# Kernel tuning notes

Measured on AMD Instinct MI355X. Metric: run time of the kernel, lower is better.

Reference implementation:

```python
import jax, jax.numpy as jnp
import numpy as np
import math

N_MENTIONS = 8192
EMB = 1024


def setup_inputs() -> dict:
    key = jax.random.key(0)
    k0, k1, k2 = jax.random.split(key, 3)
    scale = 1.0 / math.sqrt(EMB)
    return {
        "all_mentions": jax.random.normal(k0, (N_MENTIONS, EMB), dtype=jnp.float32),
        "Wq": jax.random.normal(k1, (EMB, EMB), dtype=jnp.float32) * scale,
        "bq": jnp.zeros((EMB,), dtype=jnp.float32),
        "Wk": jax.random.normal(k2, (EMB, EMB), dtype=jnp.float32) * scale,
        "bk": jnp.zeros((EMB,), dtype=jnp.float32),
    }


def reference(all_mentions, Wq, bq, Wk, bk):
    # torch.nn.Linear: y = x @ W.T + b
    E = all_mentions.shape[-1]
    q = (all_mentions @ Wq.T + bq) / jnp.sqrt(jnp.asarray(E, all_mentions.dtype))
    k = all_mentions @ Wk.T + bk
    # [N, N] raw attention logits
    attn = q @ k.T
    # causal mask: -inf strictly above the diagonal (triu, diagonal=1)
    n = all_mentions.shape[0]
    mask = jnp.where(jnp.triu(jnp.ones((n, n), dtype=bool), k=1),
                     jnp.asarray(-jnp.inf, attn.dtype),
                     jnp.asarray(0.0, attn.dtype))
    # Module returns attn_weights = masked pre-softmax logits (single layer,
    # single head, bsz=1); the softmax@v branch is discarded by the caller.
    return attn + mask
```

## Files before the change

kernel.cpp:

```cpp
#include <hip/hip_runtime.h>
#include <math.h>

#define NM 8192
#define KDIM 1024

#define NEG_BIG (-3.0e38f)

typedef __attribute__((ext_vector_type(4))) float floatx4;
typedef __attribute__((ext_vector_type(8))) _Float16 halfx8;
typedef __attribute__((ext_vector_type(4))) _Float16 halfx4;

__device__ __forceinline__ void gload_lds16(const void* g, void* l) {
    __builtin_amdgcn_global_load_lds(
        (const __attribute__((address_space(1))) void*)g,
        (__attribute__((address_space(3))) void*)l,
        16, 0, 0);
}

__global__ __launch_bounds__(256)
void convert_kernel(const float* __restrict__ X,
                    const float* __restrict__ Wq,
                    const float* __restrict__ Wk,
                    _Float16* __restrict__ Xf,
                    _Float16* __restrict__ Wqf,
                    _Float16* __restrict__ Wkf) {
    const int XB = (NM * KDIM) / 4 / 256;
    const int WB = (KDIM * KDIM) / 4 / 256;
    int b = blockIdx.x;
    const float* src;
    _Float16* dst;
    if (b < XB)            { src = X;  dst = Xf; }
    else if (b < XB + WB)  { b -= XB;       src = Wq; dst = Wqf; }
    else                   { b -= XB + WB;  src = Wk; dst = Wkf; }
    const int i = b * 256 + threadIdx.x;
    floatx4 v = ((const floatx4*)src)[i];
    halfx4 h;
    h.x = (_Float16)v.x;
    h.y = (_Float16)v.y;
    h.z = (_Float16)v.z;
    h.w = (_Float16)v.w;
    *(halfx4*)&dst[(size_t)i * 4] = h;
}


__global__ __launch_bounds__(256, 2)
void proj_kernel(const _Float16* __restrict__ Xf,
                 const _Float16* __restrict__ Wqf, const float* __restrict__ bq,
                 _Float16* __restrict__ Qf,
                 const _Float16* __restrict__ Wkf, const float* __restrict__ bk,
                 _Float16* __restrict__ Kf) {
    const bool isK = (blockIdx.z == 1);
    const _Float16* W    = isK ? Wkf : Wqf;
    const float*    bias = isK ? bk : bq;
    _Float16*       O    = isK ? Kf : Qf;
    const float scale = isK ? 1.0f : 0.03125f;

    __shared__ __attribute__((aligned(16))) _Float16 sA[256 * 64];
    __shared__ __attribute__((aligned(16))) _Float16 sB[128 * 64];

    const int t = threadIdx.x;
    const int lane = t & 63;
    const int quad = lane >> 4;
    const int l15 = lane & 15;
    const int wave = t >> 6;
    const int wr = (wave & 1) * 128;
    const int wc = (wave >> 1) * 64;

    const int row0 = blockIdx.y * 256;
    const int col0 = blockIdx.x * 128;

    const int srow = t >> 3;
    const int skoff = (((t & 7) ^ ((t >> 3) & 7)) * 8);

    floatx4 zero = {0.f, 0.f, 0.f, 0.f};
    floatx4 acc[8][4];
#pragma unroll
    for (int i = 0; i < 8; i++)
#pragma unroll
        for (int j = 0; j < 4; j++) acc[i][j] = zero;

    for (int k0 = 0; k0 < KDIM; k0 += 64) {
#pragma unroll
        for (int c = 0; c < 8; c++) {
            const int r = c * 32 + srow;
            const size_t ga = (size_t)(row0 + r) * KDIM + k0 + skoff;
            gload_lds16(Xf + ga, &sA[(c * 256 + t) * 8]);
        }
#pragma unroll
        for (int c = 0; c < 4; c++) {
            const int r = c * 32 + srow;
            const size_t gb = (size_t)(col0 + r) * KDIM + k0 + skoff;
            gload_lds16(W + gb, &sB[(c * 256 + t) * 8]);
        }
        __syncthreads();

#pragma unroll
        for (int kk = 0; kk < 2; kk++) {
            halfx8 a[8];
#pragma unroll
            for (int i = 0; i < 8; i++) {
                const int r = wr + i * 16 + l15;
                const int sl = (kk * 4 + quad) ^ (r & 7);
                a[i] = *(const halfx8*)&sA[r * 64 + sl * 8];
            }
#pragma unroll
            for (int j = 0; j < 4; j++) {
                const int r = wc + j * 16 + l15;
                const int sl = (kk * 4 + quad) ^ (r & 7);
                halfx8 b = *(const halfx8*)&sB[r * 64 + sl * 8];
#pragma unroll
                for (int i = 0; i < 8; i++)
                    acc[i][j] = __builtin_amdgcn_mfma_f32_16x16x32_f16(a[i], b, acc[i][j], 0, 0, 0);
            }
        }
        __syncthreads();
    }

#pragma unroll
    for (int i = 0; i < 8; i++)
#pragma unroll
        for (int j = 0; j < 4; j++)
#pragma unroll
            for (int r = 0; r < 4; r++) {
                const int grow = row0 + wr + i * 16 + quad * 4 + r;
                const int gcol = col0 + wc + j * 16 + l15;
                const float v = (acc[i][j][r] + bias[gcol]) * scale;
                O[(size_t)grow * KDIM + gcol] = (_Float16)v;
            }
}

__global__ __launch_bounds__(256, 2)
void attn_kernel(const _Float16* __restrict__ Qf,
                 const _Float16* __restrict__ Kf,
                 float* __restrict__ out) {
    const int lid = blockIdx.x;
    const int x = lid & 7;
    const int s = lid >> 3;
    const int bi = s & 31;
    const int bj = ((s >> 5) << 3) + x;
    const int t = threadIdx.x;

    if (bj * 128 > bi * 256 + 255) {
        const floatx4 v = {NEG_BIG, NEG_BIG, NEG_BIG, NEG_BIG};
        floatx4* o4 = (floatx4*)(out + (size_t)bi * 256 * NM + (size_t)bj * 128);
#pragma unroll
        for (int it = 0; it < 32; ++it) {
            const int idx = it * 256 + t;
            const int r = idx >> 5;
            const int c = idx & 31;
            __builtin_nontemporal_store(v, &o4[(size_t)r * (NM / 4) + c]);
        }
        return;
    }

    __shared__ __attribute__((aligned(16))) _Float16 sA[256 * 64];
    __shared__ __attribute__((aligned(16))) _Float16 sB[128 * 64];

    const int lane = t & 63;
    const int quad = lane >> 4;
    const int l15 = lane & 15;
    const int wave = t >> 6;
    const int wr = (wave & 1) * 128;
    const int wc = (wave >> 1) * 64;

    const int row0 = bi * 256;
    const int col0 = bj * 128;

    const int srow = t >> 3;
    const int skoff = (((t & 7) ^ ((t >> 3) & 7)) * 8);

    floatx4 zero = {0.f, 0.f, 0.f, 0.f};
    floatx4 acc[8][4];
#pragma unroll
    for (int i = 0; i < 8; i++)
#pragma unroll
        for (int j = 0; j < 4; j++) acc[i][j] = zero;

    for (int k0 = 0; k0 < KDIM; k0 += 64) {
#pragma unroll
        for (int c = 0; c < 8; c++) {
            const int r = c * 32 + srow;
            const size_t ga = (size_t)(row0 + r) * KDIM + k0 + skoff;
            gload_lds16(Qf + ga, &sA[(c * 256 + t) * 8]);
        }
#pragma unroll
        for (int c = 0; c < 4; c++) {
            const int r = c * 32 + srow;
            const size_t gb = (size_t)(col0 + r) * KDIM + k0 + skoff;
            gload_lds16(Kf + gb, &sB[(c * 256 + t) * 8]);
        }
        __syncthreads();

#pragma unroll
        for (int kk = 0; kk < 2; kk++) {
            halfx8 a[8];
#pragma unroll
            for (int i = 0; i < 8; i++) {
                const int r = wr + i * 16 + l15;
                const int sl = (kk * 4 + quad) ^ (r & 7);
                a[i] = *(const halfx8*)&sA[r * 64 + sl * 8];
            }
#pragma unroll
            for (int j = 0; j < 4; j++) {
                const int r = wc + j * 16 + l15;
                const int sl = (kk * 4 + quad) ^ (r & 7);
                halfx8 b = *(const halfx8*)&sB[r * 64 + sl * 8];
#pragma unroll
                for (int i = 0; i < 8; i++)
                    acc[i][j] = __builtin_amdgcn_mfma_f32_16x16x32_f16(a[i], b, acc[i][j], 0, 0, 0);
            }
        }
        __syncthreads();
    }

#pragma unroll
    for (int i = 0; i < 8; i++)
#pragma unroll
        for (int j = 0; j < 4; j++)
#pragma unroll
            for (int r = 0; r < 4; r++) {
                const int grow = row0 + wr + i * 16 + quad * 4 + r;
                const int gcol = col0 + wc + j * 16 + l15;
                const float v = (gcol <= grow) ? acc[i][j][r] : NEG_BIG;
                __builtin_nontemporal_store(v, &out[(size_t)grow * NM + gcol]);
            }
}

extern "C" void kernel_launch(void* const* d_in, const int* in_sizes, int n_in,
                              void* d_out, int out_size, void* d_ws, size_t ws_size,
                              hipStream_t stream) {
    const float* X  = (const float*)d_in[0];
    const float* Wq = (const float*)d_in[1];
    const float* bq = (const float*)d_in[2];
    const float* Wk = (const float*)d_in[3];
    const float* bk = (const float*)d_in[4];
    float* out = (float*)d_out;

    _Float16* p = (_Float16*)d_ws;
    const size_t XN = (size_t)NM * KDIM;
    const size_t WN = (size_t)KDIM * KDIM;
    _Float16* Xf  = p;  p += XN;
    _Float16* Wqf = p;  p += WN;
    _Float16* Wkf = p;  p += WN;
    _Float16* Qf  = p;  p += XN;
    _Float16* Kf  = p;  p += XN;

    const int nconv = (int)((XN + 2 * WN) / 4 / 256);
    convert_kernel<<<nconv, 256, 0, stream>>>(X, Wq, Wk, Xf, Wqf, Wkf);

    dim3 pgrid(KDIM / 128, NM / 256, 2);
    proj_kernel<<<pgrid, 256, 0, stream>>>(Xf, Wqf, bq, Qf, Wkf, bk, Kf);

    attn_kernel<<<(NM / 256) * (NM / 128), 256, 0, stream>>>(Qf, Kf, out);
}
```

Baseline: 418.9 us.

## Double-buffer LDS tiles with async prefetch in projection and attention GEMMs

Replaces the single-buffered K=64 load/compute loop with a two-stage LDS ring of K=32 tiles. The next-but-one stage is issued with global_load_lds right after fragments are read into registers, and explicit vmcnt waits and barriers replace the two __syncthreads per iteration. MFMA work is raised in priority with s_setprio, and the swizzle is adapted to 32-wide rows. The aim is to hide global-memory latency behind MFMA compute, at the cost of finer-grained iterations, more barriers, and hand-tuned waitcnt logic that must exactly match how many loads are outstanding.

```diff
diff --git a/kernel.cpp b/kernel.cpp
--- a/kernel.cpp
+++ b/kernel.cpp
@@ -43,6 +43,58 @@
 }
 
 
+#define GEMM_PIPE_BODY(APTR, BPTR)                                            \
+    auto STAGE = [&](int kt, int pb) {                                        \
+        const int k0 = kt * 32;                                               \
+        _Pragma("unroll")                                                     \
+        for (int c = 0; c < 4; c++) {               \
+            const int r = c * 64 + srow;                                      \
+            gload_lds16(APTR + (size_t)(row0 + r) * KDIM + k0 + skoff,        \
+                        &sA[pb][(c * 256 + t) * 8]);                          \
+        }                                                                     \
+        _Pragma("unroll")                                                     \
+        for (int c = 0; c < 2; c++) {               \
+            const int r = c * 64 + srow;                                      \
+            gload_lds16(BPTR + (size_t)(col0 + r) * KDIM + k0 + skoff,        \
+                        &sB[pb][(c * 256 + t) * 8]);                          \
+        }                                                                     \
+    };                                                                        \
+    STAGE(0, 0);                                                              \
+    STAGE(1, 1);                                                              \
+    asm volatile("s_waitcnt vmcnt(6)" ::: "memory");       \
+    __builtin_amdgcn_s_barrier();                                             \
+    for (int kt = 0; kt < 32; ++kt) {                                         \
+        const int pb = kt & 1;                                                \
+        halfx8 a[8], b[4];                                                    \
+        _Pragma("unroll")                                                     \
+        for (int i = 0; i < 8; i++) {                                         \
+            const int r = wr + i * 16 + l15;                                  \
+            a[i] = *(const halfx8*)&sA[pb][r * 32 + fsl];                     \
+        }                                                                     \
+        _Pragma("unroll")                                                     \
+        for (int j = 0; j < 4; j++) {                                         \
+            const int r = wc + j * 16 + l15;                                  \
+            b[j] = *(const halfx8*)&sB[pb][r * 32 + fsl];                     \
+        }                                                                     \
+        asm volatile("s_waitcnt lgkmcnt(0)" ::: "memory");                    \
+        __builtin_amdgcn_sched_barrier(0);                                    \
+        __builtin_amdgcn_s_barrier();                                         \
+        if (kt < 30) STAGE(kt + 2, pb);                                       \
+        __builtin_amdgcn_s_setprio(1);                                        \
+        _Pragma("unroll")                                                     \
+        for (int j = 0; j < 4; j++)                                           \
+            _Pragma("unroll")                                                 \
+            for (int i = 0; i < 8; i++)                                       \
+                acc[i][j] = __builtin_amdgcn_mfma_f32_16x16x32_f16(           \
+                    a[i], b[j], acc[i][j], 0, 0, 0);                          \
+        __builtin_amdgcn_s_setprio(0);                                        \
+        if (kt < 30)                                                          \
+            asm volatile("s_waitcnt vmcnt(6)" ::: "memory");                  \
+        else if (kt == 30)                                                    \
+            asm volatile("s_waitcnt vmcnt(0)" ::: "memory");                  \
+        if (kt < 31) __builtin_amdgcn_s_barrier();                            \
+    }
+
 __global__ __launch_bounds__(256, 2)
 void proj_kernel(const _Float16* __restrict__ Xf,
                  const _Float16* __restrict__ Wqf, const float* __restrict__ bq,
@@ -55,8 +107,8 @@
     _Float16*       O    = isK ? Kf : Qf;
     const float scale = isK ? 1.0f : 0.03125f;
 
-    __shared__ __attribute__((aligned(16))) _Float16 sA[256 * 64];
-    __shared__ __attribute__((aligned(16))) _Float16 sB[128 * 64];
+    __shared__ __attribute__((aligned(16))) _Float16 sA[2][256 * 32];
+    __shared__ __attribute__((aligned(16))) _Float16 sB[2][128 * 32];
 
     const int t = threadIdx.x;
     const int lane = t & 63;
@@ -69,8 +121,9 @@
     const int row0 = blockIdx.y * 256;
     const int col0 = blockIdx.x * 128;
 
-    const int srow = t >> 3;
-    const int skoff = (((t & 7) ^ ((t >> 3) & 7)) * 8);
+    const int srow = t >> 2;
+    const int skoff = (((t & 3) ^ ((t >> 3) & 3)) * 8);
+    const int fsl = (quad ^ ((l15 >> 1) & 3)) * 8;
 
     floatx4 zero = {0.f, 0.f, 0.f, 0.f};
     floatx4 acc[8][4];
@@ -79,42 +132,7 @@
 #pragma unroll
         for (int j = 0; j < 4; j++) acc[i][j] = zero;
 
-    for (int k0 = 0; k0 < KDIM; k0 += 64) {
-#pragma unroll
-        for (int c = 0; c < 8; c++) {
-            const int r = c * 32 + srow;
-            const size_t ga = (size_t)(row0 + r) * KDIM + k0 + skoff;
-            gload_lds16(Xf + ga, &sA[(c * 256 + t) * 8]);
-        }
-#pragma unroll
-        for (int c = 0; c < 4; c++) {
-            const int r = c * 32 + srow;
-            const size_t gb = (size_t)(col0 + r) * KDIM + k0 + skoff;
-            gload_lds16(W + gb, &sB[(c * 256 + t) * 8]);
-        }
-        __syncthreads();
-
-#pragma unroll
-        for (int kk = 0; kk < 2; kk++) {
-            halfx8 a[8];
-#pragma unroll
-            for (int i = 0; i < 8; i++) {
-                const int r = wr + i * 16 + l15;
-                const int sl = (kk * 4 + quad) ^ (r & 7);
-                a[i] = *(const halfx8*)&sA[r * 64 + sl * 8];
-            }
-#pragma unroll
-            for (int j = 0; j < 4; j++) {
-                const int r = wc + j * 16 + l15;
-                const int sl = (kk * 4 + quad) ^ (r & 7);
-                halfx8 b = *(const halfx8*)&sB[r * 64 + sl * 8];
-#pragma unroll
-                for (int i = 0; i < 8; i++)
-                    acc[i][j] = __builtin_amdgcn_mfma_f32_16x16x32_f16(a[i], b, acc[i][j], 0, 0, 0);
-            }
-        }
-        __syncthreads();
-    }
+    GEMM_PIPE_BODY(Xf, W)
 
 #pragma unroll
     for (int i = 0; i < 8; i++)
@@ -153,8 +171,8 @@
         return;
     }
 
-    __shared__ __attribute__((aligned(16))) _Float16 sA[256 * 64];
-    __shared__ __attribute__((aligned(16))) _Float16 sB[128 * 64];
+    __shared__ __attribute__((aligned(16))) _Float16 sA[2][256 * 32];
+    __shared__ __attribute__((aligned(16))) _Float16 sB[2][128 * 32];
 
     const int lane = t & 63;
     const int quad = lane >> 4;
@@ -166,8 +184,9 @@
     const int row0 = bi * 256;
     const int col0 = bj * 128;
 
-    const int srow = t >> 3;
-    const int skoff = (((t & 7) ^ ((t >> 3) & 7)) * 8);
+    const int srow = t >> 2;
+    const int skoff = (((t & 3) ^ ((t >> 3) & 3)) * 8);
+    const int fsl = (quad ^ ((l15 >> 1) & 3)) * 8;
 
     floatx4 zero = {0.f, 0.f, 0.f, 0.f};
     floatx4 acc[8][4];
@@ -176,42 +195,7 @@
 #pragma unroll
         for (int j = 0; j < 4; j++) acc[i][j] = zero;
 
-    for (int k0 = 0; k0 < KDIM; k0 += 64) {
-#pragma unroll
-        for (int c = 0; c < 8; c++) {
-            const int r = c * 32 + srow;
-            const size_t ga = (size_t)(row0 + r) * KDIM + k0 + skoff;
-            gload_lds16(Qf + ga, &sA[(c * 256 + t) * 8]);
-        }
-#pragma unroll
-        for (int c = 0; c < 4; c++) {
-            const int r = c * 32 + srow;
-            const size_t gb = (size_t)(col0 + r) * KDIM + k0 + skoff;
-            gload_lds16(Kf + gb, &sB[(c * 256 + t) * 8]);
-        }
-        __syncthreads();
-
-#pragma unroll
-        for (int kk = 0; kk < 2; kk++) {
-            halfx8 a[8];
-#pragma unroll
-            for (int i = 0; i < 8; i++) {
-                const int r = wr + i * 16 + l15;
-                const int sl = (kk * 4 + quad) ^ (r & 7);
-                a[i] = *(const halfx8*)&sA[r * 64 + sl * 8];
-            }
-#pragma unroll
-            for (int j = 0; j < 4; j++) {
-                const int r = wc + j * 16 + l15;
-                const int sl = (kk * 4 + quad) ^ (r & 7);
-                halfx8 b = *(const halfx8*)&sB[r * 64 + sl * 8];
-#pragma unroll
-                for (int i = 0; i < 8; i++)
-                    acc[i][j] = __builtin_amdgcn_mfma_f32_16x16x32_f16(a[i], b, acc[i][j], 0, 0, 0);
-            }
-        }
-        __syncthreads();
-    }
+    GEMM_PIPE_BODY(Qf, Kf)
 
 #pragma unroll
     for (int i = 0; i < 8; i++)
```

Result: no change. 419.7 us (+0.2%).
